# Kernel tuning notes

Hardware: AMD Instinct MI355X
Metric: run time of the kernel (lower is better)

## Reference

```python
import jax, jax.numpy as jnp
import numpy as np

NUM_CU = 100000
NUM_CI = 50000
DIM = 64
NUM_LAYERS = 3
NUM_EDGES = 1600000
EPS = 1e-8


def setup_inputs() -> dict:
    key = jax.random.key(0)
    k1, k2, k3, k4, k5 = jax.random.split(key, 5)
    user_w = jax.random.normal(k1, (NUM_CU, DIM), dtype=jnp.float32) * 0.1
    item_w = jax.random.normal(k2, (NUM_CI, DIM), dtype=jnp.float32) * 0.1
    user_delta = jnp.zeros((NUM_CU, DIM), dtype=jnp.float32)
    item_delta = jnp.zeros((NUM_CI, DIM), dtype=jnp.float32)
    edge_logit = jax.random.normal(k3, (NUM_EDGES,), dtype=jnp.float32)
    cu = jax.random.randint(k4, (NUM_EDGES,), 0, NUM_CU, dtype=jnp.int32)
    ci = jax.random.randint(k5, (NUM_EDGES,), 0, NUM_CI, dtype=jnp.int32)
    return {"user_w": user_w, "item_w": item_w, "user_delta": user_delta,
            "item_delta": item_delta, "edge_logit": edge_logit, "cu": cu, "ci": ci}


def reference(user_w, item_w, user_delta, item_delta, edge_logit, cu, ci):
    # Learnable edge weights: softplus(logit) + eps
    w = jax.nn.softplus(edge_logit) + EPS  # [E]
    # Degree normalization via segmented sums (no atomics needed)
    deg_u = jax.ops.segment_sum(w, cu, num_segments=NUM_CU)  # [NU]
    deg_i = jax.ops.segment_sum(w, ci, num_segments=NUM_CI)  # [NI]
    norm = w / (jnp.sqrt(deg_u[cu] + EPS) * jnp.sqrt(deg_i[ci] + EPS))  # [E]

    u = user_w + user_delta  # [NU, D]
    it = item_w + item_delta  # [NI, D]
    acc_u, acc_i = u, it
    nrm = norm[:, None]  # [E, 1]
    for _ in range(NUM_LAYERS):
        # gather -> weight -> scatter (bipartite LightGCN SpMM)
        u_new = jax.ops.segment_sum(it[ci] * nrm, cu, num_segments=NUM_CU)
        i_new = jax.ops.segment_sum(u[cu] * nrm, ci, num_segments=NUM_CI)
        u, it = u_new, i_new
        acc_u = acc_u + u
        acc_i = acc_i + it
    scale = 1.0 / (NUM_LAYERS + 1)
    return acc_u * scale, acc_i * scale
```

## Files before the change

### kernel.cpp

```cpp
#include <hip/hip_runtime.h>
#include <math.h>

#define EPSV 1e-8f

constexpr int CAP = 80;

__device__ inline unsigned short f2bf(float x) {
    unsigned u = __float_as_uint(x);
    unsigned r = u + 0x7FFFu + ((u >> 16) & 1u);
    return (unsigned short)(r >> 16);
}
__device__ inline float bf2f(unsigned short b) {
    return __uint_as_float(((unsigned)b) << 16);
}

__global__ void build_direct_kernel(const float* __restrict__ logit,
                                    const int* __restrict__ cu,
                                    const int* __restrict__ ci,
                                    int* __restrict__ cnt,
                                    int2* __restrict__ adj,
                                    int NU, int E) {
    int e = blockIdx.x * blockDim.x + threadIdx.x;
    if (e >= E) return;
    float x = logit[e];
    float w = fmaxf(x, 0.f) + log1pf(expf(-fabsf(x))) + EPSV;
    int wb = __float_as_int(w);
    int u  = cu[e];
    int gi = NU + ci[e];
    int pu = atomicAdd(&cnt[u], 1);
    if (pu < CAP) adj[(size_t)u * CAP + pu] = make_int2(gi, wb);
    int pi = atomicAdd(&cnt[gi], 1);
    if (pi < CAP) adj[(size_t)gi * CAP + pi] = make_int2(u, wb);
}

__global__ void deg_init_kernel(const int2* __restrict__ adj,
                                const int* __restrict__ cnt,
                                const float* __restrict__ user_w,
                                const float* __restrict__ user_d,
                                const float* __restrict__ item_w,
                                const float* __restrict__ item_d,
                                float* __restrict__ rsq,
                                float* __restrict__ sq,
                                unsigned short* __restrict__ G0,
                                int NU, int N) {
    int row  = blockIdx.x * (blockDim.x >> 6) + (threadIdx.x >> 6);
    int lane = threadIdx.x & 63;
    if (row >= N) return;
    int n = min(cnt[row], CAP);
    const int2* arow = adj + (size_t)row * CAP;
    float s = 0.f;
    if (lane < n) s = __int_as_float(arow[lane].y);
    for (int j = 64 + lane; j < n; j += 64) s += __int_as_float(arow[j].y);
    #pragma unroll
    for (int off = 1; off < 64; off <<= 1) s += __shfl_xor(s, off, 64);
    float de = s + EPSV;
    float r = rsqrtf(de);
    if (lane == 0) { rsq[row] = r; sq[row] = de * r; }
    float f;
    if (row < NU) {
        f = user_w[(size_t)row * 64 + lane] + user_d[(size_t)row * 64 + lane];
    } else {
        size_t j = (size_t)(row - NU) * 64 + lane;
        f = item_w[j] + item_d[j];
    }
    G0[(size_t)row * 64 + lane] = f2bf(r * f);
}

__global__ void __launch_bounds__(256)
gather_kernel(const int2* __restrict__ adj,
              const int* __restrict__ cnt,
              const float* __restrict__ rsq,
              const unsigned short* __restrict__ src,
              unsigned short* __restrict__ dst,
              int N) {
    int row  = blockIdx.x * (blockDim.x >> 6) + (threadIdx.x >> 6);
    int lane = threadIdx.x & 63;
    if (row >= N) return;
    int half = lane >> 5, l32 = lane & 31;

    const int2* arow = adj + (size_t)row * CAP;
    int end = min(cnt[row], CAP);
    const unsigned* s32 = (const unsigned*)src;
    float ax = 0.f, ay = 0.f;

    int j = 0;
    for (; j + 7 < end; j += 8) {
        #pragma unroll
        for (int t = 0; t < 4; ++t) {
            int2 p = arow[j + 2 * t + half];
            float w = __int_as_float(p.y);
            unsigned sv = s32[(size_t)p.x * 32 + l32];
            ax += w * bf2f((unsigned short)(sv & 0xFFFFu));
            ay += w * bf2f((unsigned short)(sv >> 16));
        }
    }
    for (; j + 1 < end; j += 2) {
        int2 p = arow[j + half];
        float w = __int_as_float(p.y);
        unsigned sv = s32[(size_t)p.x * 32 + l32];
        ax += w * bf2f((unsigned short)(sv & 0xFFFFu));
        ay += w * bf2f((unsigned short)(sv >> 16));
    }
    if (j < end) {
        int2 p = arow[j];
        float w = half ? 0.f : __int_as_float(p.y);
        unsigned sv = s32[(size_t)p.x * 32 + l32];
        ax += w * bf2f((unsigned short)(sv & 0xFFFFu));
        ay += w * bf2f((unsigned short)(sv >> 16));
    }

    ax += __shfl_xor(ax, 32, 64);
    ay += __shfl_xor(ay, 32, 64);

    float r = rsq[row];
    float f = r * r;
    if (half == 0) {
        unsigned o = ((unsigned)f2bf(ay * f) << 16) | (unsigned)f2bf(ax * f);
        ((unsigned*)dst)[(size_t)row * 32 + l32] = o;
    }
}

__global__ void __launch_bounds__(256)
gather_final_kernel(const int2* __restrict__ adj,
                    const int* __restrict__ cnt,
                    const float* __restrict__ rsq,
                    const float* __restrict__ sq,
                    const unsigned short* __restrict__ src,
                    const unsigned short* __restrict__ G1,
                    const unsigned short* __restrict__ G2,
                    const float* __restrict__ user_w,
                    const float* __restrict__ user_d,
                    const float* __restrict__ item_w,
                    const float* __restrict__ item_d,
                    float* __restrict__ out,
                    int NU, int N) {
    int row  = blockIdx.x * (blockDim.x >> 6) + (threadIdx.x >> 6);
    int lane = threadIdx.x & 63;
    if (row >= N) return;
    int half = lane >> 5, l32 = lane & 31;

    const int2* arow = adj + (size_t)row * CAP;
    int end = min(cnt[row], CAP);
    const unsigned* s32 = (const unsigned*)src;
    float ax = 0.f, ay = 0.f;

    int j = 0;
    for (; j + 7 < end; j += 8) {
        #pragma unroll
        for (int t = 0; t < 4; ++t) {
            int2 p = arow[j + 2 * t + half];
            float w = __int_as_float(p.y);
            unsigned sv = s32[(size_t)p.x * 32 + l32];
            ax += w * bf2f((unsigned short)(sv & 0xFFFFu));
            ay += w * bf2f((unsigned short)(sv >> 16));
        }
    }
    for (; j + 1 < end; j += 2) {
        int2 p = arow[j + half];
        float w = __int_as_float(p.y);
        unsigned sv = s32[(size_t)p.x * 32 + l32];
        ax += w * bf2f((unsigned short)(sv & 0xFFFFu));
        ay += w * bf2f((unsigned short)(sv >> 16));
    }
    if (j < end) {
        int2 p = arow[j];
        float w = half ? 0.f : __int_as_float(p.y);
        unsigned sv = s32[(size_t)p.x * 32 + l32];
        ax += w * bf2f((unsigned short)(sv & 0xFFFFu));
        ay += w * bf2f((unsigned short)(sv >> 16));
    }

    ax += __shfl_xor(ax, 32, 64);
    ay += __shfl_xor(ay, 32, 64);

    if (half == 0) {
        float r = rsq[row];
        float g3x = ax * r * r;
        float g3y = ay * r * r;
        size_t d2 = (size_t)row * 32 + l32;
        unsigned a1 = ((const unsigned*)G1)[d2];
        unsigned a2 = ((const unsigned*)G2)[d2];
        float s = sq[row];
        float2 wd;
        size_t fidx = (size_t)row * 64 + 2 * l32;
        if (row < NU) {
            float2 w2 = *(const float2*)(user_w + fidx);
            float2 dd = *(const float2*)(user_d + fidx);
            wd = make_float2(w2.x + dd.x, w2.y + dd.y);
        } else {
            size_t jj = fidx - (size_t)NU * 64;
            float2 w2 = *(const float2*)(item_w + jj);
            float2 dd = *(const float2*)(item_d + jj);
            wd = make_float2(w2.x + dd.x, w2.y + dd.y);
        }
        float2 o;
        o.x = 0.25f * (wd.x + s * (bf2f((unsigned short)(a1 & 0xFFFFu)) +
                                   bf2f((unsigned short)(a2 & 0xFFFFu)) + g3x));
        o.y = 0.25f * (wd.y + s * (bf2f((unsigned short)(a1 >> 16)) +
                                   bf2f((unsigned short)(a2 >> 16)) + g3y));
        *(float2*)(out + fidx) = o;
    }
}

extern "C" void kernel_launch(void* const* d_in, const int* in_sizes, int n_in,
                              void* d_out, int out_size, void* d_ws, size_t ws_size,
                              hipStream_t stream) {
    const float* user_w = (const float*)d_in[0];
    const float* item_w = (const float*)d_in[1];
    const float* user_d = (const float*)d_in[2];
    const float* item_d = (const float*)d_in[3];
    const float* logit  = (const float*)d_in[4];
    const int*   cu     = (const int*)d_in[5];
    const int*   ci     = (const int*)d_in[6];

    const int NU = in_sizes[0] / 64;
    const int NI = in_sizes[1] / 64;
    const int E  = in_sizes[4];
    const int N  = NU + NI;

    char* ws = (char*)d_ws;
    size_t off = 0;
    auto carve = [&](size_t bytes) -> void* {
        void* p = ws + off;
        off = (off + bytes + 255) & ~(size_t)255;
        return p;
    };
    int*   cnt = (int*)carve((size_t)N * 4);
    size_t zero_bytes = off;
    float* rsq = (float*)carve((size_t)N * 4);
    float* sq  = (float*)carve((size_t)N * 4);
    int2*  adj = (int2*)carve((size_t)N * CAP * 8);
    unsigned short* G0 = (unsigned short*)carve((size_t)N * 64 * 2);
    unsigned short* G1 = (unsigned short*)carve((size_t)N * 64 * 2);
    unsigned short* G2 = (unsigned short*)carve((size_t)N * 64 * 2);
    (void)ws_size;

    float* out = (float*)d_out;
    hipMemsetAsync(cnt, 0, zero_bytes, stream);

    int eblocks = (E + 255) / 256;
    build_direct_kernel<<<eblocks, 256, 0, stream>>>(logit, cu, ci, cnt, adj, NU, E);

    int rblocks = (N + 3) / 4;
    deg_init_kernel<<<rblocks, 256, 0, stream>>>(adj, cnt, user_w, user_d,
                                                 item_w, item_d, rsq, sq, G0, NU, N);

    gather_kernel<<<rblocks, 256, 0, stream>>>(adj, cnt, rsq, G0, G1, N);
    gather_kernel<<<rblocks, 256, 0, stream>>>(adj, cnt, rsq, G1, G2, N);

    gather_final_kernel<<<rblocks, 256, 0, stream>>>(adj, cnt, rsq, sq, G2, G1, G2,
                                                     user_w, user_d, item_w, item_d,
                                                     out, NU, N);
}
```

Before: 687.6 us.

## Build adjacency via sliced shared-memory histograms and widen gather to 64-bit lanes

Replaces the global-atomic adjacency build with a three-stage build. Per-chunk, per-edge-slice histograms are counted with LDS atomics, a per-row scan is taken across slices, and a fill pass writes each edge to its computed slot. The gather kernels now use quarter-wave lanes that each load 8 bytes (4 bf16 values), processing 4 edges per wave step, and the final kernel uses float4 loads and stores. The build scans the full edge list once per chunk (15 chunks × 32 slices) and needs extra workspace for slice counts and per-edge positions. In exchange it removes contended global atomics and keeps a deterministic slot order.

```diff
diff --git a/kernel.cpp b/kernel.cpp
--- a/kernel.cpp
+++ b/kernel.cpp
@@ -4,6 +4,8 @@
 #define EPSV 1e-8f
 
 constexpr int CAP = 80;
+constexpr int CHUNK_ROWS = 10240;
+constexpr int NSLICE = 32;
 
 __device__ inline unsigned short f2bf(float x) {
     unsigned u = __float_as_uint(x);
@@ -14,23 +16,70 @@
     return __uint_as_float(((unsigned)b) << 16);
 }
 
-__global__ void build_direct_kernel(const float* __restrict__ logit,
-                                    const int* __restrict__ cu,
-                                    const int* __restrict__ ci,
-                                    int* __restrict__ cnt,
-                                    int2* __restrict__ adj,
-                                    int NU, int E) {
+__global__ void __launch_bounds__(512)
+count32_kernel(const int* __restrict__ cu,
+               const int* __restrict__ ci,
+               int* __restrict__ cnt32,
+               int* __restrict__ pos_u,
+               int* __restrict__ pos_i,
+               int NU, int N, int E, int slice_e) {
+    __shared__ int h[CHUNK_ROWS];
+    int base = blockIdx.x * CHUNK_ROWS;
+    int lim  = min(CHUNK_ROWS, N - base);
+    if (lim <= 0) return;
+    for (int i = threadIdx.x; i < lim; i += 512) h[i] = 0;
+    __syncthreads();
+
+    int s  = blockIdx.y;
+    int es = s * slice_e;
+    int ee = min(E, es + slice_e);
+    for (int e = es + threadIdx.x; e < ee; e += 512) {
+        int ru = cu[e] - base;
+        if ((unsigned)ru < (unsigned)lim) pos_u[e] = atomicAdd(&h[ru], 1);
+        int ri = NU + ci[e] - base;
+        if ((unsigned)ri < (unsigned)lim) pos_i[e] = atomicAdd(&h[ri], 1);
+    }
+    __syncthreads();
+
+    int* dst = cnt32 + (size_t)s * N + base;
+    for (int i = threadIdx.x; i < lim; i += 512) dst[i] = h[i];
+}
+
+__global__ void scan32_kernel(int* __restrict__ cnt32,
+                              int* __restrict__ cnt, int N) {
+    int row = blockIdx.x * blockDim.x + threadIdx.x;
+    if (row >= N) return;
+    int run = 0;
+    #pragma unroll
+    for (int s = 0; s < NSLICE; ++s) {
+        size_t idx = (size_t)s * N + row;
+        int v = cnt32[idx];
+        cnt32[idx] = run;
+        run += v;
+    }
+    cnt[row] = run;
+}
+
+__global__ void fill_kernel(const float* __restrict__ logit,
+                            const int* __restrict__ cu,
+                            const int* __restrict__ ci,
+                            const int* __restrict__ sbase,
+                            const int* __restrict__ pos_u,
+                            const int* __restrict__ pos_i,
+                            int2* __restrict__ adj,
+                            int NU, int N, int E, int slice_e) {
     int e = blockIdx.x * blockDim.x + threadIdx.x;
     if (e >= E) return;
     float x = logit[e];
     float w = fmaxf(x, 0.f) + log1pf(expf(-fabsf(x))) + EPSV;
     int wb = __float_as_int(w);
+    int s  = e / slice_e;
     int u  = cu[e];
     int gi = NU + ci[e];
-    int pu = atomicAdd(&cnt[u], 1);
-    if (pu < CAP) adj[(size_t)u * CAP + pu] = make_int2(gi, wb);
-    int pi = atomicAdd(&cnt[gi], 1);
-    if (pi < CAP) adj[(size_t)gi * CAP + pi] = make_int2(u, wb);
+    int su = sbase[(size_t)s * N + u]  + pos_u[e];
+    int si = sbase[(size_t)s * N + gi] + pos_i[e];
+    if (su < CAP) adj[(size_t)u  * CAP + su] = make_int2(gi, wb);
+    if (si < CAP) adj[(size_t)gi * CAP + si] = make_int2(u,  wb);
 }
 
 __global__ void deg_init_kernel(const int2* __restrict__ adj,
@@ -76,47 +125,50 @@
     int row  = blockIdx.x * (blockDim.x >> 6) + (threadIdx.x >> 6);
     int lane = threadIdx.x & 63;
     if (row >= N) return;
-    int half = lane >> 5, l32 = lane & 31;
+    int qw = lane >> 4, l16 = lane & 15;
 
     const int2* arow = adj + (size_t)row * CAP;
     int end = min(cnt[row], CAP);
-    const unsigned* s32 = (const unsigned*)src;
-    float ax = 0.f, ay = 0.f;
+    const uint2* s64 = (const uint2*)src;
+    float a0 = 0.f, a1 = 0.f, a2 = 0.f, a3 = 0.f;
 
     int j = 0;
     for (; j + 7 < end; j += 8) {
         #pragma unroll
-        for (int t = 0; t < 4; ++t) {
-            int2 p = arow[j + 2 * t + half];
+        for (int t = 0; t < 2; ++t) {
+            int2 p = arow[j + 4 * t + qw];
             float w = __int_as_float(p.y);
-            unsigned sv = s32[(size_t)p.x * 32 + l32];
-            ax += w * bf2f((unsigned short)(sv & 0xFFFFu));
-            ay += w * bf2f((unsigned short)(sv >> 16));
+            uint2 sv = s64[(size_t)p.x * 16 + l16];
+            a0 += w * bf2f((unsigned short)(sv.x & 0xFFFFu));
+            a1 += w * bf2f((unsigned short)(sv.x >> 16));
+            a2 += w * bf2f((unsigned short)(sv.y & 0xFFFFu));
+            a3 += w * bf2f((unsigned short)(sv.y >> 16));
         }
     }
-    for (; j + 1 < end; j += 2) {
-        int2 p = arow[j + half];
-        float w = __int_as_float(p.y);
-        unsigned sv = s32[(size_t)p.x * 32 + l32];
-        ax += w * bf2f((unsigned short)(sv & 0xFFFFu));
-        ay += w * bf2f((unsigned short)(sv >> 16));
-    }
-    if (j < end) {
-        int2 p = arow[j];
-        float w = half ? 0.f : __int_as_float(p.y);
-        unsigned sv = s32[(size_t)p.x * 32 + l32];
-        ax += w * bf2f((unsigned short)(sv & 0xFFFFu));
-        ay += w * bf2f((unsigned short)(sv >> 16));
-    }
-
-    ax += __shfl_xor(ax, 32, 64);
-    ay += __shfl_xor(ay, 32, 64);
-
-    float r = rsq[row];
-    float f = r * r;
-    if (half == 0) {
-        unsigned o = ((unsigned)f2bf(ay * f) << 16) | (unsigned)f2bf(ax * f);
-        ((unsigned*)dst)[(size_t)row * 32 + l32] = o;
+    for (; j < end; j += 4) {
+        int idx = j + qw;
+        bool v = idx < end;
+        int2 p = arow[v ? idx : (end - 1)];
+        float w = v ? __int_as_float(p.y) : 0.f;
+        uint2 sv = s64[(size_t)p.x * 16 + l16];
+        a0 += w * bf2f((unsigned short)(sv.x & 0xFFFFu));
+        a1 += w * bf2f((unsigned short)(sv.x >> 16));
+        a2 += w * bf2f((unsigned short)(sv.y & 0xFFFFu));
+        a3 += w * bf2f((unsigned short)(sv.y >> 16));
+    }
+
+    a0 += __shfl_xor(a0, 16, 64); a0 += __shfl_xor(a0, 32, 64);
+    a1 += __shfl_xor(a1, 16, 64); a1 += __shfl_xor(a1, 32, 64);
+    a2 += __shfl_xor(a2, 16, 64); a2 += __shfl_xor(a2, 32, 64);
+    a3 += __shfl_xor(a3, 16, 64); a3 += __shfl_xor(a3, 32, 64);
+
+    if (qw == 0) {
+        float r = rsq[row];
+        float f = r * r;
+        uint2 o;
+        o.x = ((unsigned)f2bf(a1 * f) << 16) | (unsigned)f2bf(a0 * f);
+        o.y = ((unsigned)f2bf(a3 * f) << 16) | (unsigned)f2bf(a2 * f);
+        ((uint2*)dst)[(size_t)row * 16 + l16] = o;
     }
 }
 
@@ -137,68 +189,71 @@
     int row  = blockIdx.x * (blockDim.x >> 6) + (threadIdx.x >> 6);
     int lane = threadIdx.x & 63;
     if (row >= N) return;
-    int half = lane >> 5, l32 = lane & 31;
+    int qw = lane >> 4, l16 = lane & 15;
 
     const int2* arow = adj + (size_t)row * CAP;
     int end = min(cnt[row], CAP);
-    const unsigned* s32 = (const unsigned*)src;
-    float ax = 0.f, ay = 0.f;
+    const uint2* s64 = (const uint2*)src;
+    float a0 = 0.f, a1 = 0.f, a2 = 0.f, a3 = 0.f;
 
     int j = 0;
     for (; j + 7 < end; j += 8) {
         #pragma unroll
-        for (int t = 0; t < 4; ++t) {
-            int2 p = arow[j + 2 * t + half];
+        for (int t = 0; t < 2; ++t) {
+            int2 p = arow[j + 4 * t + qw];
             float w = __int_as_float(p.y);
-            unsigned sv = s32[(size_t)p.x * 32 + l32];
-            ax += w * bf2f((unsigned short)(sv & 0xFFFFu));
-            ay += w * bf2f((unsigned short)(sv >> 16));
+            uint2 sv = s64[(size_t)p.x * 16 + l16];
+            a0 += w * bf2f((unsigned short)(sv.x & 0xFFFFu));
+            a1 += w * bf2f((unsigned short)(sv.x >> 16));
+            a2 += w * bf2f((unsigned short)(sv.y & 0xFFFFu));
+            a3 += w * bf2f((unsigned short)(sv.y >> 16));
         }
     }
-    for (; j + 1 < end; j += 2) {
-        int2 p = arow[j + half];
-        float w = __int_as_float(p.y);
-        unsigned sv = s32[(size_t)p.x * 32 + l32];
-        ax += w * bf2f((unsigned short)(sv & 0xFFFFu));
-        ay += w * bf2f((unsigned short)(sv >> 16));
-    }
-    if (j < end) {
-        int2 p = arow[j];
-        float w = half ? 0.f : __int_as_float(p.y);
-        unsigned sv = s32[(size_t)p.x * 32 + l32];
-        ax += w * bf2f((unsigned short)(sv & 0xFFFFu));
-        ay += w * bf2f((unsigned short)(sv >> 16));
-    }
-
-    ax += __shfl_xor(ax, 32, 64);
-    ay += __shfl_xor(ay, 32, 64);
-
-    if (half == 0) {
+    for (; j < end; j += 4) {
+        int idx = j + qw;
+        bool v = idx < end;
+        int2 p = arow[v ? idx : (end - 1)];
+        float w = v ? __int_as_float(p.y) : 0.f;
+        uint2 sv = s64[(size_t)p.x * 16 + l16];
+        a0 += w * bf2f((unsigned short)(sv.x & 0xFFFFu));
+        a1 += w * bf2f((unsigned short)(sv.x >> 16));
+        a2 += w * bf2f((unsigned short)(sv.y & 0xFFFFu));
+        a3 += w * bf2f((unsigned short)(sv.y >> 16));
+    }
+
+    a0 += __shfl_xor(a0, 16, 64); a0 += __shfl_xor(a0, 32, 64);
+    a1 += __shfl_xor(a1, 16, 64); a1 += __shfl_xor(a1, 32, 64);
+    a2 += __shfl_xor(a2, 16, 64); a2 += __shfl_xor(a2, 32, 64);
+    a3 += __shfl_xor(a3, 16, 64); a3 += __shfl_xor(a3, 32, 64);
+
+    if (qw == 0) {
         float r = rsq[row];
-        float g3x = ax * r * r;
-        float g3y = ay * r * r;
-        size_t d2 = (size_t)row * 32 + l32;
-        unsigned a1 = ((const unsigned*)G1)[d2];
-        unsigned a2 = ((const unsigned*)G2)[d2];
+        float f = r * r;
+        float g3_0 = a0 * f, g3_1 = a1 * f, g3_2 = a2 * f, g3_3 = a3 * f;
+        size_t d2 = (size_t)row * 16 + l16;
+        uint2 b1 = ((const uint2*)G1)[d2];
+        uint2 b2 = ((const uint2*)G2)[d2];
         float s = sq[row];
-        float2 wd;
-        size_t fidx = (size_t)row * 64 + 2 * l32;
+        size_t fidx = (size_t)row * 64 + 4 * l16;
+        float4 w4, d4;
         if (row < NU) {
-            float2 w2 = *(const float2*)(user_w + fidx);
-            float2 dd = *(const float2*)(user_d + fidx);
-            wd = make_float2(w2.x + dd.x, w2.y + dd.y);
+            w4 = *(const float4*)(user_w + fidx);
+            d4 = *(const float4*)(user_d + fidx);
         } else {
             size_t jj = fidx - (size_t)NU * 64;
-            float2 w2 = *(const float2*)(item_w + jj);
-            float2 dd = *(const float2*)(item_d + jj);
-            wd = make_float2(w2.x + dd.x, w2.y + dd.y);
+            w4 = *(const float4*)(item_w + jj);
+            d4 = *(const float4*)(item_d + jj);
         }
-        float2 o;
-        o.x = 0.25f * (wd.x + s * (bf2f((unsigned short)(a1 & 0xFFFFu)) +
-                                   bf2f((unsigned short)(a2 & 0xFFFFu)) + g3x));
-        o.y = 0.25f * (wd.y + s * (bf2f((unsigned short)(a1 >> 16)) +
-                                   bf2f((unsigned short)(a2 >> 16)) + g3y));
-        *(float2*)(out + fidx) = o;
+        float4 o;
+        o.x = 0.25f * (w4.x + d4.x + s * (bf2f((unsigned short)(b1.x & 0xFFFFu)) +
+                                          bf2f((unsigned short)(b2.x & 0xFFFFu)) + g3_0));
+        o.y = 0.25f * (w4.y + d4.y + s * (bf2f((unsigned short)(b1.x >> 16)) +
+                                          bf2f((unsigned short)(b2.x >> 16)) + g3_1));
+        o.z = 0.25f * (w4.z + d4.z + s * (bf2f((unsigned short)(b1.y & 0xFFFFu)) +
+                                          bf2f((unsigned short)(b2.y & 0xFFFFu)) + g3_2));
+        o.w = 0.25f * (w4.w + d4.w + s * (bf2f((unsigned short)(b1.y >> 16)) +
+                                          bf2f((unsigned short)(b2.y >> 16)) + g3_3));
+        *(float4*)(out + fidx) = o;
     }
 }
 
@@ -217,6 +272,8 @@
     const int NI = in_sizes[1] / 64;
     const int E  = in_sizes[4];
     const int N  = NU + NI;
+    const int NCHUNK  = (N + CHUNK_ROWS - 1) / CHUNK_ROWS;
+    const int slice_e = (E + NSLICE - 1) / NSLICE;
 
     char* ws = (char*)d_ws;
     size_t off = 0;
@@ -225,21 +282,26 @@
         off = (off + bytes + 255) & ~(size_t)255;
         return p;
     };
-    int*   cnt = (int*)carve((size_t)N * 4);
-    size_t zero_bytes = off;
-    float* rsq = (float*)carve((size_t)N * 4);
-    float* sq  = (float*)carve((size_t)N * 4);
-    int2*  adj = (int2*)carve((size_t)N * CAP * 8);
+    int*   cnt32 = (int*)carve((size_t)NSLICE * N * 4);
+    int*   cnt   = (int*)carve((size_t)N * 4);
+    float* rsq   = (float*)carve((size_t)N * 4);
+    float* sq    = (float*)carve((size_t)N * 4);
+    int*   pos_u = (int*)carve((size_t)E * 4);
+    int*   pos_i = (int*)carve((size_t)E * 4);
+    int2*  adj   = (int2*)carve((size_t)N * CAP * 8);
     unsigned short* G0 = (unsigned short*)carve((size_t)N * 64 * 2);
     unsigned short* G1 = (unsigned short*)carve((size_t)N * 64 * 2);
     unsigned short* G2 = (unsigned short*)carve((size_t)N * 64 * 2);
     (void)ws_size;
 
     float* out = (float*)d_out;
-    hipMemsetAsync(cnt, 0, zero_bytes, stream);
-
+
+    count32_kernel<<<dim3(NCHUNK, NSLICE), 512, 0, stream>>>(
+        cu, ci, cnt32, pos_u, pos_i, NU, N, E, slice_e);
+    scan32_kernel<<<(N + 255) / 256, 256, 0, stream>>>(cnt32, cnt, N);
     int eblocks = (E + 255) / 256;
-    build_direct_kernel<<<eblocks, 256, 0, stream>>>(logit, cu, ci, cnt, adj, NU, E);
+    fill_kernel<<<eblocks, 256, 0, stream>>>(logit, cu, ci, cnt32, pos_u, pos_i,
+                                             adj, NU, N, E, slice_e);
 
     int rblocks = (N + 3) / 4;
     deg_init_kernel<<<rblocks, 256, 0, stream>>>(adj, cnt, user_w, user_d,
```

After: 615.3 us. -10.5%, faster.
